# Kernel optimization log

Measured on AMD Instinct MI355X. Metric: run time of the kernel, lower is better.

The kernel has to match this reference:

```python
import jax, jax.numpy as jnp
import numpy as np

DIMENSIONS = 10000
NUM_LEVELS = 500
NUM_CLASSES = 128
SIZE = 6
BATCH = 256
MAX_TEMPERATURE = 41.6
MIN_TEMPERATURE = -19.9


def setup_inputs() -> dict:
    key = jax.random.key(0)
    k_x, k_w, k_b, k_r, k_c = jax.random.split(key, 5)
    x = jax.random.normal(k_x, (BATCH, SIZE), dtype=jnp.float32)
    # Sinusoid projection params: weight [D, size] ~ N(0,1), bias [D] ~ U(0, 2*pi)
    W_proj = jax.random.normal(k_w, (DIMENSIONS, SIZE), dtype=jnp.float32)
    b_proj = jax.random.uniform(k_b, (DIMENSIONS,), dtype=jnp.float32) * (2.0 * np.pi)
    W_reg = jax.random.normal(k_r, (NUM_CLASSES, DIMENSIONS), dtype=jnp.float32)
    # Level codebook: bipolar +-1 hypervectors [500, D]
    codebook = jnp.where(jax.random.normal(k_c, (NUM_LEVELS, DIMENSIONS)) > 0, 1.0, -1.0).astype(jnp.float32)
    return {"x": x, "W_proj": W_proj, "b_proj": b_proj, "W_reg": W_reg, "codebook": codebook}


def reference(x, W_proj, b_proj, W_reg, codebook):
    # Sinusoid projection: cos(xW^T + b) * sin(xW^T)  -> [B, D]
    proj = x @ W_proj.T
    sample_hv = jnp.cos(proj + b_proj) * jnp.sin(proj)
    # hard_quantize: sign to {+1, -1}
    enc = jnp.where(sample_hv > 0, 1.0, -1.0).astype(x.dtype)
    # bind(W_reg, enc) -> [B, C, D]; dot_similarity with codebook -> [B, C, K].
    # Fused as a single trilinear contraction (avoids the B*C*D intermediate).
    sim = jnp.einsum('bd,cd,kd->bck', enc, W_reg, codebook)
    index = jnp.argmax(sim, axis=-1)  # [B, C]
    slope = MAX_TEMPERATURE - MIN_TEMPERATURE
    pred = index.astype(jnp.float32) / (NUM_LEVELS - 1) * slope + MIN_TEMPERATURE
    return pred
```

## Files before the change

kernel.cpp:

```cpp
#include <hip/hip_runtime.h>
#include <math.h>

#define B_SZ 256
#define S_SZ 6
#define D_SZ 10000
#define DP   10112
#define C_SZ 128
#define K_SZ 500
#define KP   512
#define NIT  (DP / 64)
#define THR  1.0f
#define RCAP 32768

typedef _Float16       half8 __attribute__((ext_vector_type(8)));
typedef float          f32x4 __attribute__((ext_vector_type(4)));
typedef unsigned int   u32x4v __attribute__((ext_vector_type(4)));
typedef unsigned short u16x4 __attribute__((ext_vector_type(4)));
typedef unsigned int   u32x4b __attribute__((ext_vector_type(4)));

__device__ __forceinline__ void stage16(const void* g, void* l) {
    __builtin_amdgcn_global_load_lds(
        (const __attribute__((address_space(1))) unsigned int*)g,
        (__attribute__((address_space(3))) unsigned int*)l, 16, 0, 0);
}

__global__ void prep_fused(const float* __restrict__ cb, _Float16* __restrict__ cbp,
                           const float* __restrict__ wreg, _Float16* __restrict__ whi,
                           const float* __restrict__ x, const float* __restrict__ wp,
                           const float* __restrict__ bp, unsigned short* __restrict__ em,
                           int* __restrict__ counter) {
    if (blockIdx.x == 0 && threadIdx.x == 0) *counter = 0;
    int t = blockIdx.x * 256 + threadIdx.x;
    if (t < KP * DP) {
        int k = t / DP, d = t - k * DP;
        float v = (k < K_SZ && d < D_SZ) ? cb[k * D_SZ + d] : 0.0f;
        cbp[t] = (_Float16)v;
    }
    if (t < C_SZ * DP) {
        int c = t / DP, d = t - c * DP;
        float w = (d < D_SZ) ? wreg[c * D_SZ + d] : 0.0f;
        whi[t] = (_Float16)w;
    }
    if (t < B_SZ * DP) {
        int b = t / DP, d = t - b * DP;
        unsigned short m = 0;
        if (d < D_SZ) {
            double p = 0.0;
            #pragma unroll
            for (int s = 0; s < S_SZ; ++s)
                p += (double)x[b * S_SZ + s] * (double)wp[d * S_SZ + s];
            const double inv2pi = 0.15915494309189535;
            double t1 = p * inv2pi;
            double f1 = t1 - floor(t1);
            double t2 = (p + (double)bp[d]) * inv2pi;
            double f2 = t2 - floor(t2);
            bool sin_pos = (f1 < 0.5);
            bool cos_pos = (f2 < 0.25) || (f2 > 0.75);
            m = (sin_pos == cos_pos) ? (unsigned short)0u : (unsigned short)0x8000u;
        }
        em[t] = m;
    }
}

__global__ __launch_bounds__(256, 2) void gemm_sim(
    const _Float16* __restrict__ whi, const _Float16* __restrict__ cbp,
    const unsigned short* __restrict__ em, _Float16* __restrict__ simh)
{
    const int kt = blockIdx.x >> 1;
    const int ct = blockIdx.x & 1;
    const int bg = blockIdx.y;
    const int tid  = threadIdx.x;
    const int wave = tid >> 6;
    const int lane = tid & 63;
    const int quad = lane >> 4;
    const int col  = lane & 15;

    __shared__ __align__(16) _Float16 s_whi[2][64 * 64];
    __shared__ __align__(16) _Float16 s_cb [2][64 * 64];
    __shared__ __align__(16) unsigned short s_mask[2][8 * 64];

    f32x4 acc[2][4][4];
    #pragma unroll
    for (int b = 0; b < 2; ++b)
        #pragma unroll
        for (int m = 0; m < 4; ++m)
            #pragma unroll
            for (int n = 0; n < 4; ++n)
                acc[b][m][n] = (f32x4){0.f, 0.f, 0.f, 0.f};

    const int c0  = ct * 64;
    const int kr0 = kt * 64;
    const int bg8 = bg * 8;

    size_t abase[2], bbase[2];
    int soff[2];
    #pragma unroll
    for (int s = 0; s < 2; ++s) {
        int e = s * 256 + tid;
        int row = e >> 3;
        int p = e & 7;
        int gcol = (p ^ (row & 7)) * 8;
        abase[s] = (size_t)(c0 + row) * DP + gcol;
        bbase[s] = (size_t)(kr0 + row) * DP + gcol;
        soff[s] = e * 8;
    }
    const size_t embase = (size_t)(bg8 + (tid >> 3)) * DP + (tid & 7) * 8;

    auto STAGE = [&](int buf, int kb) {
        const int k0 = kb * 64;
        #pragma unroll
        for (int s = 0; s < 2; ++s) {
            stage16(whi + abase[s] + k0, &s_whi[buf][soff[s]]);
            stage16(cbp + bbase[s] + k0, &s_cb [buf][soff[s]]);
        }
        if (tid < 64)
            stage16(em + embase + k0, &s_mask[buf][tid * 8]);
    };

    STAGE(0, 0);
    __syncthreads();
    int cur = 0;

    for (int kb = 0; kb < NIT; ++kb) {
        if (kb + 1 < NIT) STAGE(cur ^ 1, kb + 1);

        u32x4v ah[2][4], br[2][4], mr[2][2];
        #pragma unroll
        for (int k2 = 0; k2 < 2; ++k2) {
            const int chunk = k2 * 4 + quad;
            const int sw    = (chunk ^ (col & 7)) * 8;
            #pragma unroll
            for (int m = 0; m < 4; ++m)
                ah[k2][m] = *(const u32x4v*)(&s_whi[cur][(m * 16 + col) * 64 + sw]);
            #pragma unroll
            for (int n = 0; n < 4; ++n)
                br[k2][n] = *(const u32x4v*)(&s_cb[cur][(n * 16 + col) * 64 + sw]);
            #pragma unroll
            for (int b = 0; b < 2; ++b)
                mr[k2][b] = *(const u32x4v*)(&s_mask[cur][(wave * 2 + b) * 64 + chunk * 8]);
        }
        #pragma unroll
        for (int k2 = 0; k2 < 2; ++k2) {
            #pragma unroll
            for (int b = 0; b < 2; ++b) {
                half8 bs[4];
                #pragma unroll
                for (int n = 0; n < 4; ++n)
                    bs[n] = __builtin_bit_cast(half8, br[k2][n] ^ mr[k2][b]);
                #pragma unroll
                for (int m = 0; m < 4; ++m) {
                    half8 a = __builtin_bit_cast(half8, ah[k2][m]);
                    #pragma unroll
                    for (int n = 0; n < 4; ++n)
                        acc[b][m][n] = __builtin_amdgcn_mfma_f32_16x16x32_f16(a, bs[n], acc[b][m][n], 0, 0, 0);
                }
            }
        }
        __syncthreads();
        cur ^= 1;
    }

    #pragma unroll
    for (int b = 0; b < 2; ++b) {
        const size_t base = ((size_t)(bg8 + wave * 2 + b) * C_SZ + (size_t)c0) * KP;
        #pragma unroll
        for (int m = 0; m < 4; ++m)
            #pragma unroll
            for (int n = 0; n < 4; ++n) {
                const int kg = kr0 + n * 16 + col;
                #pragma unroll
                for (int r = 0; r < 4; ++r) {
                    const int cl = m * 16 + quad * 4 + r;
                    simh[base + (size_t)cl * KP + kg] = (_Float16)acc[b][m][n][r];
                }
            }
    }
}

__global__ __launch_bounds__(256) void argmax_gap(
    const _Float16* __restrict__ simh, float* __restrict__ out,
    int* __restrict__ counter, int* __restrict__ list)
{
    const int wave = threadIdx.x >> 6, lane = threadIdx.x & 63;
    const int row = blockIdx.x * 4 + wave;
    const half8 v = *(const half8*)(simh + (size_t)row * KP + lane * 8);
    float bv = -3.0e38f, bv2 = -3.0e38f; int bk = 0x7fffffff;
    #pragma unroll
    for (int j = 0; j < 8; ++j) {
        const int k = lane * 8 + j;
        const float f = (k < K_SZ) ? (float)v[j] : -3.0e38f;
        if (f > bv)       { bv2 = bv; bv = f; bk = k; }
        else if (f > bv2) { bv2 = f; }
    }
    #pragma unroll
    for (int off = 1; off < 64; off <<= 1) {
        const float ov  = __shfl_xor(bv,  off, 64);
        const int   ok  = __shfl_xor(bk,  off, 64);
        const float ov2 = __shfl_xor(bv2, off, 64);
        if (ov > bv || (ov == bv && ok < bk)) { bv2 = fmaxf(bv, ov2); bv = ov; bk = ok; }
        else                                  { bv2 = fmaxf(ov, bv2); }
    }
    if (lane == 0) {
        out[row] = (float)bk * (61.5f / 499.0f) - 19.9f;
        if (bv - bv2 < THR) {
            const int idx = atomicAdd(counter, 1);
            if (idx < RCAP) list[idx] = row;
        }
    }
}

__global__ __launch_bounds__(256) void repair(
    const _Float16* __restrict__ simh, const int* __restrict__ list,
    const int* __restrict__ counter, const unsigned short* __restrict__ em,
    const float* __restrict__ wreg, const _Float16* __restrict__ cbp,
    float* __restrict__ out)
{
    const int wave = threadIdx.x >> 6, lane = threadIdx.x & 63;
    const int wid = blockIdx.x * 4 + wave;
    const int nw  = gridDim.x * 4;
    int n = *counter;
    if (n > RCAP) n = RCAP;
    for (int i = wid; i < n; i += nw) {
        const int row = list[i];
        const int b = row >> 7, c = row & 127;
        const half8 v = *(const half8*)(simh + (size_t)row * KP + lane * 8);
        float vf[8];
        float mx = -3.0e38f;
        #pragma unroll
        for (int j = 0; j < 8; ++j) {
            const int k = lane * 8 + j;
            vf[j] = (k < K_SZ) ? (float)v[j] : -3.0e38f;
            mx = fmaxf(mx, vf[j]);
        }
        #pragma unroll
        for (int off = 1; off < 64; off <<= 1)
            mx = fmaxf(mx, __shfl_xor(mx, off, 64));
        const float thr = mx - THR;

        const float* wr = wreg + (size_t)c * D_SZ;
        const unsigned short* eb = em + (size_t)b * DP;

        double best = -1.0e300; int bestk = 0x7fffffff;
        #pragma unroll
        for (int j = 0; j < 8; ++j) {
            unsigned long long bal = __ballot(vf[j] >= thr);
            while (bal) {
                const int l = __ffsll((long long)bal) - 1;
                bal &= bal - 1;
                const int k = l * 8 + j;
                const unsigned short* ck = (const unsigned short*)(cbp + (size_t)k * DP);
                double s0 = 0.0, s1 = 0.0, s2 = 0.0, s3 = 0.0;
                for (int d = lane * 4; d < D_SZ; d += 256) {
                    const f32x4 w  = *(const f32x4*)(wr + d);
                    const u16x4 e4 = *(const u16x4*)(eb + d);
                    const u16x4 c4 = *(const u16x4*)(ck + d);
                    const u32x4b wb = __builtin_bit_cast(u32x4b, w);
                    u32x4b sb;
                    #pragma unroll
                    for (int q = 0; q < 4; ++q)
                        sb[q] = wb[q] ^ ((unsigned int)((e4[q] ^ c4[q]) & 0x8000u) << 16);
                    const f32x4 ws = __builtin_bit_cast(f32x4, sb);
                    s0 += (double)ws[0];
                    s1 += (double)ws[1];
                    s2 += (double)ws[2];
                    s3 += (double)ws[3];
                }
                double s = (s0 + s1) + (s2 + s3);
                #pragma unroll
                for (int off = 1; off < 64; off <<= 1)
                    s += __shfl_xor(s, off, 64);
                if (s > best || (s == best && k < bestk)) { best = s; bestk = k; }
            }
        }
        if (lane == 0)
            out[row] = (float)bestk * (61.5f / 499.0f) - 19.9f;
    }
}

extern "C" void kernel_launch(void* const* d_in, const int* in_sizes, int n_in,
                              void* d_out, int out_size, void* d_ws, size_t ws_size,
                              hipStream_t stream) {
    const float* x    = (const float*)d_in[0];
    const float* wp   = (const float*)d_in[1];
    const float* bp   = (const float*)d_in[2];
    const float* wreg = (const float*)d_in[3];
    const float* cb   = (const float*)d_in[4];
    float* out = (float*)d_out;

    char* ws = (char*)d_ws;
    size_t o = 0;
    auto take = [&](size_t bytes) -> char* {
        o = (o + 255) & ~(size_t)255;
        char* p = ws + o;
        o += bytes;
        return p;
    };
    _Float16* whi       = (_Float16*)take(sizeof(_Float16) * C_SZ * DP);
    _Float16* cbp       = (_Float16*)take(sizeof(_Float16) * KP * DP);
    unsigned short* em  = (unsigned short*)take(sizeof(unsigned short) * B_SZ * DP);
    _Float16* simh      = (_Float16*)take(sizeof(_Float16) * (size_t)B_SZ * C_SZ * KP);
    int* counter        = (int*)take(sizeof(int));
    int* list           = (int*)take(sizeof(int) * RCAP);
    (void)ws_size; (void)in_sizes; (void)n_in; (void)out_size;

    prep_fused<<<(KP * DP + 255) / 256, 256, 0, stream>>>(
        cb, cbp, wreg, whi, x, wp, bp, em, counter);

    dim3 g(16, 32);
    gemm_sim<<<g, 256, 0, stream>>>(whi, cbp, em, simh);

    argmax_gap<<<(B_SZ * C_SZ) / 4, 256, 0, stream>>>(simh, out, counter, list);
    repair<<<1024, 256, 0, stream>>>(simh, list, counter, em, wreg, cbp, out);
}
```

Before: 366.2 us.

## Switch GEMM to 32x32x16 MFMA with register double-buffered LDS reads; vectorize prep

The similarity GEMM moves from 16x16x32 MFMA tiles to 32x32x16 tiles, which means fewer LDS fragment loads per FLOP. It also software-pipelines the LDS-to-register fragment loads across four k-substeps, and the epilogue index mapping is changed to match the 32x32 accumulator layout. The prep kernel is restructured into a 2D grid where each thread converts or computes 8 contiguous elements with vector loads and stores, instead of one element per thread with integer division. The larger accumulator tiles raise register pressure, and the new lane mapping must be correct for the swizzled LDS layout.

```diff
diff --git a/kernel.cpp b/kernel.cpp
--- a/kernel.cpp
+++ b/kernel.cpp
@@ -14,8 +14,10 @@
 
 typedef _Float16       half8 __attribute__((ext_vector_type(8)));
 typedef float          f32x4 __attribute__((ext_vector_type(4)));
+typedef float          f32x16 __attribute__((ext_vector_type(16)));
 typedef unsigned int   u32x4v __attribute__((ext_vector_type(4)));
 typedef unsigned short u16x4 __attribute__((ext_vector_type(4)));
+typedef unsigned short u16x8 __attribute__((ext_vector_type(8)));
 typedef unsigned int   u32x4b __attribute__((ext_vector_type(4)));
 
 __device__ __forceinline__ void stage16(const void* g, void* l) {
@@ -29,36 +31,70 @@
                            const float* __restrict__ x, const float* __restrict__ wp,
                            const float* __restrict__ bp, unsigned short* __restrict__ em,
                            int* __restrict__ counter) {
-    if (blockIdx.x == 0 && threadIdx.x == 0) *counter = 0;
-    int t = blockIdx.x * 256 + threadIdx.x;
-    if (t < KP * DP) {
-        int k = t / DP, d = t - k * DP;
-        float v = (k < K_SZ && d < D_SZ) ? cb[k * D_SZ + d] : 0.0f;
-        cbp[t] = (_Float16)v;
-    }
-    if (t < C_SZ * DP) {
-        int c = t / DP, d = t - c * DP;
-        float w = (d < D_SZ) ? wreg[c * D_SZ + d] : 0.0f;
-        whi[t] = (_Float16)w;
-    }
-    if (t < B_SZ * DP) {
-        int b = t / DP, d = t - b * DP;
-        unsigned short m = 0;
-        if (d < D_SZ) {
-            double p = 0.0;
-            #pragma unroll
-            for (int s = 0; s < S_SZ; ++s)
-                p += (double)x[b * S_SZ + s] * (double)wp[d * S_SZ + s];
-            const double inv2pi = 0.15915494309189535;
-            double t1 = p * inv2pi;
-            double f1 = t1 - floor(t1);
-            double t2 = (p + (double)bp[d]) * inv2pi;
-            double f2 = t2 - floor(t2);
-            bool sin_pos = (f1 < 0.5);
-            bool cos_pos = (f2 < 0.25) || (f2 > 0.75);
-            m = (sin_pos == cos_pos) ? (unsigned short)0u : (unsigned short)0x8000u;
-        }
-        em[t] = m;
+    if (blockIdx.x == 0 && blockIdx.y == 0 && threadIdx.x == 0) *counter = 0;
+    const int d = blockIdx.x * 2048 + threadIdx.x * 8;
+    if (d >= DP) return;
+    const int y = blockIdx.y;
+    if (y < KP) {
+        const int k = y;
+        half8 hv;
+        if (k < K_SZ && d + 8 <= D_SZ) {
+            const f32x4 v0 = *(const f32x4*)(cb + (size_t)k * D_SZ + d);
+            const f32x4 v1 = *(const f32x4*)(cb + (size_t)k * D_SZ + d + 4);
+            #pragma unroll
+            for (int j = 0; j < 4; ++j) { hv[j] = (_Float16)v0[j]; hv[4 + j] = (_Float16)v1[j]; }
+        } else {
+            #pragma unroll
+            for (int j = 0; j < 8; ++j)
+                hv[j] = (_Float16)((k < K_SZ && d + j < D_SZ) ? cb[(size_t)k * D_SZ + d + j] : 0.0f);
+        }
+        *(half8*)(cbp + (size_t)k * DP + d) = hv;
+    } else if (y < KP + C_SZ) {
+        const int c = y - KP;
+        half8 hv;
+        if (d + 8 <= D_SZ) {
+            const f32x4 v0 = *(const f32x4*)(wreg + (size_t)c * D_SZ + d);
+            const f32x4 v1 = *(const f32x4*)(wreg + (size_t)c * D_SZ + d + 4);
+            #pragma unroll
+            for (int j = 0; j < 4; ++j) { hv[j] = (_Float16)v0[j]; hv[4 + j] = (_Float16)v1[j]; }
+        } else {
+            #pragma unroll
+            for (int j = 0; j < 8; ++j)
+                hv[j] = (_Float16)((d + j < D_SZ) ? wreg[(size_t)c * D_SZ + d + j] : 0.0f);
+        }
+        *(half8*)(whi + (size_t)c * DP + d) = hv;
+    } else {
+        const int b = y - KP - C_SZ;
+        u16x8 mv;
+        if (d + 8 <= D_SZ) {
+            float xv[S_SZ];
+            #pragma unroll
+            for (int s = 0; s < S_SZ; ++s) xv[s] = x[b * S_SZ + s];
+            float wv[48];
+            const float* wpd = wp + (size_t)d * S_SZ;
+            #pragma unroll
+            for (int q = 0; q < 12; ++q)
+                *(f32x4*)(wv + q * 4) = *(const f32x4*)(wpd + q * 4);
+            #pragma unroll
+            for (int j = 0; j < 8; ++j) {
+                double p = 0.0;
+                #pragma unroll
+                for (int s = 0; s < S_SZ; ++s)
+                    p += (double)xv[s] * (double)wv[j * S_SZ + s];
+                const double inv2pi = 0.15915494309189535;
+                double t1 = p * inv2pi;
+                double f1 = t1 - floor(t1);
+                double t2 = (p + (double)bp[d + j]) * inv2pi;
+                double f2 = t2 - floor(t2);
+                bool sin_pos = (f1 < 0.5);
+                bool cos_pos = (f2 < 0.25) || (f2 > 0.75);
+                mv[j] = (sin_pos == cos_pos) ? (unsigned short)0u : (unsigned short)0x8000u;
+            }
+        } else {
+            #pragma unroll
+            for (int j = 0; j < 8; ++j) mv[j] = 0;
+        }
+        *(u16x8*)(em + (size_t)b * DP + d) = mv;
     }
 }
 
@@ -72,21 +108,24 @@
     const int tid  = threadIdx.x;
     const int wave = tid >> 6;
     const int lane = tid & 63;
-    const int quad = lane >> 4;
-    const int col  = lane & 15;
+    const int hi   = lane >> 5;
+    const int l31  = lane & 31;
+    const int swz  = lane & 7;
 
     __shared__ __align__(16) _Float16 s_whi[2][64 * 64];
     __shared__ __align__(16) _Float16 s_cb [2][64 * 64];
     __shared__ __align__(16) unsigned short s_mask[2][8 * 64];
 
-    f32x4 acc[2][4][4];
+    f32x16 acc[2][2][2];
     #pragma unroll
     for (int b = 0; b < 2; ++b)
         #pragma unroll
-        for (int m = 0; m < 4; ++m)
-            #pragma unroll
-            for (int n = 0; n < 4; ++n)
-                acc[b][m][n] = (f32x4){0.f, 0.f, 0.f, 0.f};
+        for (int m = 0; m < 2; ++m)
+            #pragma unroll
+            for (int n = 0; n < 2; ++n)
+                #pragma unroll
+                for (int r = 0; r < 16; ++r)
+                    acc[b][m][n][r] = 0.f;
 
     const int c0  = ct * 64;
     const int kr0 = kt * 64;
@@ -124,35 +163,52 @@
     for (int kb = 0; kb < NIT; ++kb) {
         if (kb + 1 < NIT) STAGE(cur ^ 1, kb + 1);
 
-        u32x4v ah[2][4], br[2][4], mr[2][2];
-        #pragma unroll
-        for (int k2 = 0; k2 < 2; ++k2) {
-            const int chunk = k2 * 4 + quad;
-            const int sw    = (chunk ^ (col & 7)) * 8;
-            #pragma unroll
-            for (int m = 0; m < 4; ++m)
-                ah[k2][m] = *(const u32x4v*)(&s_whi[cur][(m * 16 + col) * 64 + sw]);
-            #pragma unroll
-            for (int n = 0; n < 4; ++n)
-                br[k2][n] = *(const u32x4v*)(&s_cb[cur][(n * 16 + col) * 64 + sw]);
+        const _Float16* ba = &s_whi[cur][0];
+        const _Float16* bb = &s_cb [cur][0];
+        const unsigned short* bm = &s_mask[cur][wave * 2 * 64];
+
+        u32x4v ah[2][2], br[2][2], mr[2][2];
+        {
+            const int ch0 = (hi ^ swz) * 8;
+            #pragma unroll
+            for (int m = 0; m < 2; ++m)
+                ah[0][m] = *(const u32x4v*)(ba + (m * 32 + l31) * 64 + ch0);
+            #pragma unroll
+            for (int n = 0; n < 2; ++n)
+                br[0][n] = *(const u32x4v*)(bb + (n * 32 + l31) * 64 + ch0);
             #pragma unroll
             for (int b = 0; b < 2; ++b)
-                mr[k2][b] = *(const u32x4v*)(&s_mask[cur][(wave * 2 + b) * 64 + chunk * 8]);
-        }
-        #pragma unroll
-        for (int k2 = 0; k2 < 2; ++k2) {
+                mr[0][b] = *(const u32x4v*)(bm + b * 64 + hi * 8);
+        }
+        #pragma unroll
+        for (int ks = 0; ks < 4; ++ks) {
+            const int st = ks & 1;
+            if (ks < 3) {
+                const int nst = st ^ 1;
+                const int ch = (((ks + 1) * 2 + hi) ^ swz) * 8;
+                #pragma unroll
+                for (int m = 0; m < 2; ++m)
+                    ah[nst][m] = *(const u32x4v*)(ba + (m * 32 + l31) * 64 + ch);
+                #pragma unroll
+                for (int n = 0; n < 2; ++n)
+                    br[nst][n] = *(const u32x4v*)(bb + (n * 32 + l31) * 64 + ch);
+                #pragma unroll
+                for (int b = 0; b < 2; ++b)
+                    mr[nst][b] = *(const u32x4v*)(bm + b * 64 + (ks + 1) * 16 + hi * 8);
+            }
             #pragma unroll
             for (int b = 0; b < 2; ++b) {
-                half8 bs[4];
-                #pragma unroll
-                for (int n = 0; n < 4; ++n)
-                    bs[n] = __builtin_bit_cast(half8, br[k2][n] ^ mr[k2][b]);
-                #pragma unroll
-                for (int m = 0; m < 4; ++m) {
-                    half8 a = __builtin_bit_cast(half8, ah[k2][m]);
+                half8 bs[2];
+                #pragma unroll
+                for (int n = 0; n < 2; ++n)
+                    bs[n] = __builtin_bit_cast(half8, br[st][n] ^ mr[st][b]);
+                #pragma unroll
+                for (int m = 0; m < 2; ++m) {
+                    half8 a = __builtin_bit_cast(half8, ah[st][m]);
                     #pragma unroll
-                    for (int n = 0; n < 4; ++n)
-                        acc[b][m][n] = __builtin_amdgcn_mfma_f32_16x16x32_f16(a, bs[n], acc[b][m][n], 0, 0, 0);
+                    for (int n = 0; n < 2; ++n)
+                        acc[b][m][n] = __builtin_amdgcn_mfma_f32_32x32x16_f16(
+                            a, bs[n], acc[b][m][n], 0, 0, 0);
                 }
             }
         }
@@ -164,13 +220,13 @@
     for (int b = 0; b < 2; ++b) {
         const size_t base = ((size_t)(bg8 + wave * 2 + b) * C_SZ + (size_t)c0) * KP;
         #pragma unroll
-        for (int m = 0; m < 4; ++m)
-            #pragma unroll
-            for (int n = 0; n < 4; ++n) {
-                const int kg = kr0 + n * 16 + col;
-                #pragma unroll
-                for (int r = 0; r < 4; ++r) {
-                    const int cl = m * 16 + quad * 4 + r;
+        for (int m = 0; m < 2; ++m)
+            #pragma unroll
+            for (int n = 0; n < 2; ++n) {
+                const int kg = kr0 + n * 32 + l31;
+                #pragma unroll
+                for (int r = 0; r < 16; ++r) {
+                    const int cl = m * 32 + (r & 3) + 8 * (r >> 2) + 4 * hi;
                     simh[base + (size_t)cl * KP + kg] = (_Float16)acc[b][m][n][r];
                 }
             }
@@ -303,8 +359,8 @@
     int* list           = (int*)take(sizeof(int) * RCAP);
     (void)ws_size; (void)in_sizes; (void)n_in; (void)out_size;
 
-    prep_fused<<<(KP * DP + 255) / 256, 256, 0, stream>>>(
-        cb, cbp, wreg, whi, x, wp, bp, em, counter);
+    dim3 gp(5, KP + C_SZ + B_SZ);
+    prep_fused<<<gp, 256, 0, stream>>>(cb, cbp, wreg, whi, x, wp, bp, em, counter);
 
     dim3 g(16, 32);
     gemm_sim<<<g, 256, 0, stream>>>(whi, cbp, em, simh);
```

Measured after the change: 393.1 us. 1.07x slower.

## Vectorize prep kernel and fuse argmax with inline exact repair

Applied to the files above, without the earlier changes.

The prep kernel is reorganised so each thread handles 8 contiguous elements over a 2D grid (row kind by blockIdx.y), using vector float loads and half8/u16x8 stores instead of one element per thread with integer divisions. The argmax and repair kernels are merged: each wave checks its own gap and, for near-tie rows, runs the exact double-precision recheck in place. This removes the atomic counter, the list buffer and one kernel launch. The repair now reads sign bits from the fp32 codebook directly. The cost is that inline repair adds divergence and load imbalance to waves with ambiguous rows.

```diff
diff --git a/kernel.cpp b/kernel.cpp
--- a/kernel.cpp
+++ b/kernel.cpp
@@ -10,12 +10,12 @@
 #define KP   512
 #define NIT  (DP / 64)
 #define THR  1.0f
-#define RCAP 32768
 
 typedef _Float16       half8 __attribute__((ext_vector_type(8)));
 typedef float          f32x4 __attribute__((ext_vector_type(4)));
 typedef unsigned int   u32x4v __attribute__((ext_vector_type(4)));
 typedef unsigned short u16x4 __attribute__((ext_vector_type(4)));
+typedef unsigned short u16x8 __attribute__((ext_vector_type(8)));
 typedef unsigned int   u32x4b __attribute__((ext_vector_type(4)));
 
 __device__ __forceinline__ void stage16(const void* g, void* l) {
@@ -27,38 +27,70 @@
 __global__ void prep_fused(const float* __restrict__ cb, _Float16* __restrict__ cbp,
                            const float* __restrict__ wreg, _Float16* __restrict__ whi,
                            const float* __restrict__ x, const float* __restrict__ wp,
-                           const float* __restrict__ bp, unsigned short* __restrict__ em,
-                           int* __restrict__ counter) {
-    if (blockIdx.x == 0 && threadIdx.x == 0) *counter = 0;
-    int t = blockIdx.x * 256 + threadIdx.x;
-    if (t < KP * DP) {
-        int k = t / DP, d = t - k * DP;
-        float v = (k < K_SZ && d < D_SZ) ? cb[k * D_SZ + d] : 0.0f;
-        cbp[t] = (_Float16)v;
-    }
-    if (t < C_SZ * DP) {
-        int c = t / DP, d = t - c * DP;
-        float w = (d < D_SZ) ? wreg[c * D_SZ + d] : 0.0f;
-        whi[t] = (_Float16)w;
-    }
-    if (t < B_SZ * DP) {
-        int b = t / DP, d = t - b * DP;
-        unsigned short m = 0;
-        if (d < D_SZ) {
-            double p = 0.0;
-            #pragma unroll
-            for (int s = 0; s < S_SZ; ++s)
-                p += (double)x[b * S_SZ + s] * (double)wp[d * S_SZ + s];
-            const double inv2pi = 0.15915494309189535;
-            double t1 = p * inv2pi;
-            double f1 = t1 - floor(t1);
-            double t2 = (p + (double)bp[d]) * inv2pi;
-            double f2 = t2 - floor(t2);
-            bool sin_pos = (f1 < 0.5);
-            bool cos_pos = (f2 < 0.25) || (f2 > 0.75);
-            m = (sin_pos == cos_pos) ? (unsigned short)0u : (unsigned short)0x8000u;
-        }
-        em[t] = m;
+                           const float* __restrict__ bp, unsigned short* __restrict__ em) {
+    const int d = blockIdx.x * 2048 + threadIdx.x * 8;
+    if (d >= DP) return;
+    const int y = blockIdx.y;
+    if (y < KP) {
+        const int k = y;
+        half8 hv;
+        if (k < K_SZ && d + 8 <= D_SZ) {
+            const f32x4 v0 = *(const f32x4*)(cb + (size_t)k * D_SZ + d);
+            const f32x4 v1 = *(const f32x4*)(cb + (size_t)k * D_SZ + d + 4);
+            #pragma unroll
+            for (int j = 0; j < 4; ++j) { hv[j] = (_Float16)v0[j]; hv[4 + j] = (_Float16)v1[j]; }
+        } else {
+            #pragma unroll
+            for (int j = 0; j < 8; ++j)
+                hv[j] = (_Float16)((k < K_SZ && d + j < D_SZ) ? cb[(size_t)k * D_SZ + d + j] : 0.0f);
+        }
+        *(half8*)(cbp + (size_t)k * DP + d) = hv;
+    } else if (y < KP + C_SZ) {
+        const int c = y - KP;
+        half8 hv;
+        if (d + 8 <= D_SZ) {
+            const f32x4 v0 = *(const f32x4*)(wreg + (size_t)c * D_SZ + d);
+            const f32x4 v1 = *(const f32x4*)(wreg + (size_t)c * D_SZ + d + 4);
+            #pragma unroll
+            for (int j = 0; j < 4; ++j) { hv[j] = (_Float16)v0[j]; hv[4 + j] = (_Float16)v1[j]; }
+        } else {
+            #pragma unroll
+            for (int j = 0; j < 8; ++j)
+                hv[j] = (_Float16)((d + j < D_SZ) ? wreg[(size_t)c * D_SZ + d + j] : 0.0f);
+        }
+        *(half8*)(whi + (size_t)c * DP + d) = hv;
+    } else {
+        const int b = y - KP - C_SZ;
+        u16x8 mv;
+        if (d + 8 <= D_SZ) {
+            float xv[S_SZ];
+            #pragma unroll
+            for (int s = 0; s < S_SZ; ++s) xv[s] = x[b * S_SZ + s];
+            float wv[48];
+            const float* wpd = wp + (size_t)d * S_SZ;
+            #pragma unroll
+            for (int q = 0; q < 12; ++q)
+                *(f32x4*)(wv + q * 4) = *(const f32x4*)(wpd + q * 4);
+            #pragma unroll
+            for (int j = 0; j < 8; ++j) {
+                double p = 0.0;
+                #pragma unroll
+                for (int s = 0; s < S_SZ; ++s)
+                    p += (double)xv[s] * (double)wv[j * S_SZ + s];
+                const double inv2pi = 0.15915494309189535;
+                double t1 = p * inv2pi;
+                double f1 = t1 - floor(t1);
+                double t2 = (p + (double)bp[d + j]) * inv2pi;
+                double f2 = t2 - floor(t2);
+                bool sin_pos = (f1 < 0.5);
+                bool cos_pos = (f2 < 0.25) || (f2 > 0.75);
+                mv[j] = (sin_pos == cos_pos) ? (unsigned short)0u : (unsigned short)0x8000u;
+            }
+        } else {
+            #pragma unroll
+            for (int j = 0; j < 8; ++j) mv[j] = 0;
+        }
+        *(u16x8*)(em + (size_t)b * DP + d) = mv;
     }
 }
 
@@ -177,20 +209,22 @@
     }
 }
 
-__global__ __launch_bounds__(256) void argmax_gap(
-    const _Float16* __restrict__ simh, float* __restrict__ out,
-    int* __restrict__ counter, int* __restrict__ list)
+__global__ __launch_bounds__(256) void argmax_repair(
+    const _Float16* __restrict__ simh, const unsigned short* __restrict__ em,
+    const float* __restrict__ wreg, const float* __restrict__ cb,
+    float* __restrict__ out)
 {
     const int wave = threadIdx.x >> 6, lane = threadIdx.x & 63;
     const int row = blockIdx.x * 4 + wave;
     const half8 v = *(const half8*)(simh + (size_t)row * KP + lane * 8);
+    float vf[8];
     float bv = -3.0e38f, bv2 = -3.0e38f; int bk = 0x7fffffff;
     #pragma unroll
     for (int j = 0; j < 8; ++j) {
         const int k = lane * 8 + j;
-        const float f = (k < K_SZ) ? (float)v[j] : -3.0e38f;
-        if (f > bv)       { bv2 = bv; bv = f; bk = k; }
-        else if (f > bv2) { bv2 = f; }
+        vf[j] = (k < K_SZ) ? (float)v[j] : -3.0e38f;
+        if (vf[j] > bv)       { bv2 = bv; bv = vf[j]; bk = k; }
+        else if (vf[j] > bv2) { bv2 = vf[j]; }
     }
     #pragma unroll
     for (int off = 1; off < 64; off <<= 1) {
@@ -200,47 +234,14 @@
         if (ov > bv || (ov == bv && ok < bk)) { bv2 = fmaxf(bv, ov2); bv = ov; bk = ok; }
         else                                  { bv2 = fmaxf(ov, bv2); }
     }
-    if (lane == 0) {
-        out[row] = (float)bk * (61.5f / 499.0f) - 19.9f;
-        if (bv - bv2 < THR) {
-            const int idx = atomicAdd(counter, 1);
-            if (idx < RCAP) list[idx] = row;
-        }
-    }
-}
-
-__global__ __launch_bounds__(256) void repair(
-    const _Float16* __restrict__ simh, const int* __restrict__ list,
-    const int* __restrict__ counter, const unsigned short* __restrict__ em,
-    const float* __restrict__ wreg, const _Float16* __restrict__ cbp,
-    float* __restrict__ out)
-{
-    const int wave = threadIdx.x >> 6, lane = threadIdx.x & 63;
-    const int wid = blockIdx.x * 4 + wave;
-    const int nw  = gridDim.x * 4;
-    int n = *counter;
-    if (n > RCAP) n = RCAP;
-    for (int i = wid; i < n; i += nw) {
-        const int row = list[i];
+
+    int bestk = bk;
+    if (bv - bv2 < THR) {
         const int b = row >> 7, c = row & 127;
-        const half8 v = *(const half8*)(simh + (size_t)row * KP + lane * 8);
-        float vf[8];
-        float mx = -3.0e38f;
-        #pragma unroll
-        for (int j = 0; j < 8; ++j) {
-            const int k = lane * 8 + j;
-            vf[j] = (k < K_SZ) ? (float)v[j] : -3.0e38f;
-            mx = fmaxf(mx, vf[j]);
-        }
-        #pragma unroll
-        for (int off = 1; off < 64; off <<= 1)
-            mx = fmaxf(mx, __shfl_xor(mx, off, 64));
-        const float thr = mx - THR;
-
+        const float thr = bv - THR;
         const float* wr = wreg + (size_t)c * D_SZ;
         const unsigned short* eb = em + (size_t)b * DP;
-
-        double best = -1.0e300; int bestk = 0x7fffffff;
+        double best = -1.0e300; bestk = 0x7fffffff;
         #pragma unroll
         for (int j = 0; j < 8; ++j) {
             unsigned long long bal = __ballot(vf[j] >= thr);
@@ -248,17 +249,18 @@
                 const int l = __ffsll((long long)bal) - 1;
                 bal &= bal - 1;
                 const int k = l * 8 + j;
-                const unsigned short* ck = (const unsigned short*)(cbp + (size_t)k * DP);
+                const float* ck = cb + (size_t)k * D_SZ;
                 double s0 = 0.0, s1 = 0.0, s2 = 0.0, s3 = 0.0;
                 for (int d = lane * 4; d < D_SZ; d += 256) {
                     const f32x4 w  = *(const f32x4*)(wr + d);
                     const u16x4 e4 = *(const u16x4*)(eb + d);
-                    const u16x4 c4 = *(const u16x4*)(ck + d);
+                    const f32x4 cw = *(const f32x4*)(ck + d);
                     const u32x4b wb = __builtin_bit_cast(u32x4b, w);
+                    const u32x4b cbits = __builtin_bit_cast(u32x4b, cw);
                     u32x4b sb;
                     #pragma unroll
                     for (int q = 0; q < 4; ++q)
-                        sb[q] = wb[q] ^ ((unsigned int)((e4[q] ^ c4[q]) & 0x8000u) << 16);
+                        sb[q] = wb[q] ^ ((((unsigned int)e4[q] << 16) ^ cbits[q]) & 0x80000000u);
                     const f32x4 ws = __builtin_bit_cast(f32x4, sb);
                     s0 += (double)ws[0];
                     s1 += (double)ws[1];
@@ -272,9 +274,9 @@
                 if (s > best || (s == best && k < bestk)) { best = s; bestk = k; }
             }
         }
-        if (lane == 0)
-            out[row] = (float)bestk * (61.5f / 499.0f) - 19.9f;
-    }
+    }
+    if (lane == 0)
+        out[row] = (float)bestk * (61.5f / 499.0f) - 19.9f;
 }
 
 extern "C" void kernel_launch(void* const* d_in, const int* in_sizes, int n_in,
@@ -299,16 +301,13 @@
     _Float16* cbp       = (_Float16*)take(sizeof(_Float16) * KP * DP);
     unsigned short* em  = (unsigned short*)take(sizeof(unsigned short) * B_SZ * DP);
     _Float16* simh      = (_Float16*)take(sizeof(_Float16) * (size_t)B_SZ * C_SZ * KP);
-    int* counter        = (int*)take(sizeof(int));
-    int* list           = (int*)take(sizeof(int) * RCAP);
     (void)ws_size; (void)in_sizes; (void)n_in; (void)out_size;
 
-    prep_fused<<<(KP * DP + 255) / 256, 256, 0, stream>>>(
-        cb, cbp, wreg, whi, x, wp, bp, em, counter);
+    dim3 gp(5, KP + C_SZ + B_SZ);
+    prep_fused<<<gp, 256, 0, stream>>>(cb, cbp, wreg, whi, x, wp, bp, em);
 
     dim3 g(16, 32);
     gemm_sim<<<g, 256, 0, stream>>>(whi, cbp, em, simh);
 
-    argmax_gap<<<(B_SZ * C_SZ) / 4, 256, 0, stream>>>(simh, out, counter, list);
-    repair<<<1024, 256, 0, stream>>>(simh, list, counter, em, wreg, cbp, out);
-}
+    argmax_repair<<<(B_SZ * C_SZ) / 4, 256, 0, stream>>>(simh, em, wreg, cb, out);
+}
```

Measured after the change: 355.5 us (median of 2 runs). -2.9%, faster.
